# Optimization experiments

Measured on AMD Instinct MI355X. Metric: run time of the kernel, lower is better.

Reference implementation:

```python
import math
import jax, jax.numpy as jnp
import numpy as np

B, L, D, H = 4, 1024, 512, 8
DK = D // H

def setup_inputs() -> dict:
    key = jax.random.key(0)
    ks = jax.random.split(key, 12)
    s = 0.02
    return {
        "query": jax.random.normal(ks[0], (B, L, D), jnp.float32),
        "key": jax.random.normal(ks[1], (B, L, D), jnp.float32),
        "value": jax.random.normal(ks[2], (B, L, D), jnp.float32),
        "wq_w": jax.random.normal(ks[3], (D, D), jnp.float32) * s,
        "wq_b": jnp.zeros((D,), jnp.float32),
        "wk_w": jax.random.normal(ks[4], (D, D), jnp.float32) * s,
        "wk_b": jnp.zeros((D,), jnp.float32),
        "wv_w": jax.random.normal(ks[5], (D, D), jnp.float32) * s,
        "wv_b": jnp.zeros((D,), jnp.float32),
        "dense_w": jax.random.normal(ks[6], (D, D), jnp.float32) * s,
        "dense_b": jnp.zeros((D,), jnp.float32),
        "gate_w": jax.random.normal(ks[7], (D, 1), jnp.float32) * s,
        "gate_b": jnp.zeros((1,), jnp.float32),
        "mp_wq_w": jax.random.normal(ks[8], (D, D), jnp.float32) * s,
        "mp_wq_b": jnp.zeros((D,), jnp.float32),
        "mp_wk_w": jax.random.normal(ks[9], (D, D), jnp.float32) * s,
        "mp_wk_b": jnp.zeros((D,), jnp.float32),
    }

def reference(query, key, value, wq_w, wq_b, wk_w, wk_b, wv_w, wv_b,
              dense_w, dense_b, gate_w, gate_b,
              mp_wq_w, mp_wq_b, mp_wk_w, mp_wk_b):
    # Multi-head projections -> (B, H, L, DK)
    q = (query @ wq_w + wq_b).reshape(B, L, H, DK).transpose(0, 2, 1, 3)
    k = (key @ wk_w + wk_b).reshape(B, L, H, DK).transpose(0, 2, 1, 3)
    v = (value @ wv_w + wv_b).reshape(B, L, H, DK).transpose(0, 2, 1, 3)

    # MaskPerturbation on original (unprojected-into-heads) Q, K; scale by sqrt(d_model)
    qp = query @ mp_wq_w + mp_wq_b              # (B, L, D)
    kp = key @ mp_wk_w + mp_wk_b                # (B, L, D)
    m = jax.nn.sigmoid(jnp.einsum('bqd,bkd->bqk', qp, kp) / math.sqrt(D))  # (B, L, L)

    # Scaled dot-product attention (no mask)
    scores = jnp.einsum('bhqd,bhkd->bhqk', q, k) / math.sqrt(DK)  # (B, H, L, L)
    p_attn = jax.nn.softmax(scores, axis=-1)

    # Calibration: attn_cal = attn * exp(1 - m), combined with per-query gate, re-softmax
    attn_cal = p_attn * jnp.exp(1.0 - m[:, None])                 # (B, H, L, L)
    g = jax.nn.sigmoid(query @ gate_w + gate_b)[:, None]          # (B, 1, L, 1)
    attn_comb = g * p_attn + (1.0 - g) * attn_cal
    attn_final = jax.nn.softmax(attn_comb, axis=-1)

    out = jnp.einsum('bhqk,bhkd->bhqd', attn_final, v)            # (B, H, L, DK)
    out = out.transpose(0, 2, 1, 3).reshape(B, L, D)
    out = out @ dense_w + dense_b                                 # dropout p=0 (eval)
    return (out, m)
```

## Files before the change

### kernel.cpp

```cpp
#include <hip/hip_runtime.h>

#define B_  4
#define L_  1024
#define D_  512
#define H_  8
#define DK_ 64
#define BL_ (B_*L_)

typedef unsigned short us16;
typedef __attribute__((ext_vector_type(8))) short bf16x8;
typedef __attribute__((ext_vector_type(4))) float f32x4;

__device__ __forceinline__ float us2f(us16 u) {
  union { unsigned int i; float f; } x;
  x.i = ((unsigned int)u) << 16;
  return x.f;
}
__device__ __forceinline__ us16 f2us(float f) {
  union { float f; unsigned int i; } x;
  x.f = f;
  unsigned int r = x.i + 0x7FFFu + ((x.i >> 16) & 1u);
  return (us16)(r >> 16);
}
__device__ __forceinline__ us16 cvt_us(float f) { return f2us(f); }
__device__ __forceinline__ us16 cvt_us(us16 u) { return u; }
__device__ __forceinline__ float fexp2(float x) {
  return __builtin_amdgcn_exp2f(x);
}

#define MFMA(a, b, c) __builtin_amdgcn_mfma_f32_16x16x32_bf16(a, b, c, 0, 0, 0)

struct WT6 {
  const float* src[6];
  us16* dst[6];
};
__global__ __launch_bounds__(256) void prep(WT6 p, const float* __restrict__ query,
    const float* __restrict__ gw, const float* __restrict__ gb,
    float* __restrict__ g, us16* __restrict__ qb) {
  __shared__ us16 T[64][72];
  int id = blockIdx.x;
  const int t = threadIdx.x;
  if (id < 1024) {
    int row = id * 4 + (t >> 6);
    int lane = t & 63;
    float pz = 0.f;
    for (int d = lane; d < D_; d += 64) pz += query[(size_t)row * D_ + d] * gw[d];
#pragma unroll
    for (int off = 32; off; off >>= 1) pz += __shfl_down(pz, off);
    if (lane == 0) g[row] = 1.f / (1.f + __expf(-(pz + gb[0])));
    return;
  }
  if (id >= 1408) {
    size_t base = (size_t)(id - 1408) * 4096 + t * 16;
    const float* src = query + base;
    union { bf16x8 v; us16 u[8]; } a0, a1;
#pragma unroll
    for (int j = 0; j < 8; ++j) { a0.u[j] = f2us(src[j]); a1.u[j] = f2us(src[8 + j]); }
    *(bf16x8*)&qb[base] = a0.v;
    *(bf16x8*)&qb[base + 8] = a1.v;
    return;
  }
  id -= 1024;
  const int z = id >> 6;
  const int k0 = ((id >> 3) & 7) * 64, n0 = (id & 7) * 64;
  const float* __restrict__ W = p.src[z];
  us16* __restrict__ Wt = p.dst[z];
  {
    int r = t >> 2, c = (t & 3) * 16;
    const float* src = W + (size_t)(k0 + r) * 512 + n0 + c;
    union { bf16x8 v; us16 u[8]; } p0, p1;
#pragma unroll
    for (int j = 0; j < 8; ++j) { p0.u[j] = f2us(src[j]); p1.u[j] = f2us(src[8 + j]); }
    *(bf16x8*)&T[r][c] = p0.v;
    *(bf16x8*)&T[r][c + 8] = p1.v;
  }
  __syncthreads();
  {
    int n = t >> 2, c = (t & 3) * 16;
    union { bf16x8 v; us16 u[8]; } p0, p1;
#pragma unroll
    for (int j = 0; j < 8; ++j) { p0.u[j] = T[c + j][n]; p1.u[j] = T[c + 8 + j][n]; }
    us16* dst = Wt + (size_t)(n0 + n) * 512 + k0 + c;
    *(bf16x8*)dst = p0.v;
    *(bf16x8*)(dst + 8) = p1.v;
  }
}

__global__ __launch_bounds__(256) void gate_kernel(
    const float* __restrict__ query, const float* __restrict__ gw,
    const float* __restrict__ gb, float* __restrict__ g) {
  int row = blockIdx.x * 4 + (threadIdx.x >> 6);
  int lane = threadIdx.x & 63;
  float p = 0.f;
  for (int d = lane; d < D_; d += 64) p += query[(size_t)row * D_ + d] * gw[d];
#pragma unroll
  for (int off = 32; off; off >>= 1) p += __shfl_down(p, off);
  if (lane == 0) g[row] = 1.f / (1.f + __expf(-(p + gb[0])));
}

struct GJob {
  const float* A; const us16* Ab; const us16* Wt;
  const float* bias; us16* C; int mode; int atype;
};
struct GJobs { GJob j[3]; };

__global__ __launch_bounds__(256) void gemm3(GJobs jobs) {
  __shared__ us16 Al[64][72];
  __shared__ us16 Wl[64][72];
  int f = blockIdx.x + 8 * (blockIdx.y + 64 * blockIdx.z);
  const int cpx = 64 * (int)gridDim.z;
  f = (f & 7) * cpx + (f >> 3);
  const int bx = f & 7, by = (f >> 3) & 63, bz = f >> 9;
  const GJob J = jobs.j[bz];
  const int tid = threadIdx.x;
  const int w = tid >> 6, lane = tid & 63;
  const int quad = lane >> 4, lc = lane & 15;
  const int row0 = by * 64, col0 = bx * 64;
  const int sr = tid >> 2, sc = (tid & 3) * 16;
  f32x4 acc[4] = {};
  for (int k0 = 0; k0 < 512; k0 += 64) {
    if (J.atype) {
      const us16* as = J.Ab + (size_t)(row0 + sr) * 512 + k0 + sc;
      *(bf16x8*)&Al[sr][sc] = *(const bf16x8*)as;
      *(bf16x8*)&Al[sr][sc + 8] = *(const bf16x8*)(as + 8);
    } else {
      const float* as = J.A + (size_t)(row0 + sr) * 512 + k0 + sc;
      union { bf16x8 v; us16 u[8]; } p0, p1;
#pragma unroll
      for (int j = 0; j < 8; ++j) { p0.u[j] = f2us(as[j]); p1.u[j] = f2us(as[8 + j]); }
      *(bf16x8*)&Al[sr][sc] = p0.v;
      *(bf16x8*)&Al[sr][sc + 8] = p1.v;
    }
    {
      const us16* wsrc = J.Wt + (size_t)(col0 + sr) * 512 + k0 + sc;
      *(bf16x8*)&Wl[sr][sc] = *(const bf16x8*)wsrc;
      *(bf16x8*)&Wl[sr][sc + 8] = *(const bf16x8*)(wsrc + 8);
    }
    __syncthreads();
    bf16x8 a0 = *(const bf16x8*)&Al[w * 16 + lc][quad * 8];
    bf16x8 a1 = *(const bf16x8*)&Al[w * 16 + lc][32 + quad * 8];
#pragma unroll
    for (int ct = 0; ct < 4; ++ct) {
      bf16x8 b0 = *(const bf16x8*)&Wl[ct * 16 + lc][quad * 8];
      bf16x8 b1 = *(const bf16x8*)&Wl[ct * 16 + lc][32 + quad * 8];
      acc[ct] = MFMA(a0, b0, acc[ct]);
      acc[ct] = MFMA(a1, b1, acc[ct]);
    }
    __syncthreads();
  }
  const int orow = row0 + w * 16 + quad * 4;
#pragma unroll
  for (int ct = 0; ct < 4; ++ct) {
    const int col = col0 + ct * 16 + lc;
    const float bv = J.bias[col];
    if (J.mode == 0) {
#pragma unroll
      for (int r = 0; r < 4; ++r)
        J.C[(size_t)(orow + r) * 512 + col] = f2us(acc[ct][r] + bv);
    } else {
      const int h = col >> 6, dk = col & 63;
#pragma unroll
      for (int r = 0; r < 4; ++r) {
        const int grow = orow + r;
        const int b = grow >> 10, kv = grow & 1023;
        J.C[(((size_t)b * H_ + h) * DK_ + dk) * L_ + kv] = f2us(acc[ct][r] + bv);
      }
    }
  }
}

__global__ __launch_bounds__(256) void gemm_dense(
    const us16* __restrict__ A, const us16* __restrict__ Wt,
    const float* __restrict__ bias, float* __restrict__ C) {
  __shared__ us16 Al[64][72];
  __shared__ us16 Wl[64][72];
  int f = blockIdx.x + 8 * blockIdx.y;
  f = (f & 7) * 64 + (f >> 3);
  const int bx = f & 7, by = f >> 3;
  const int tid = threadIdx.x;
  const int w = tid >> 6, lane = tid & 63;
  const int quad = lane >> 4, lc = lane & 15;
  const int row0 = by * 64, col0 = bx * 64;
  const int sr = tid >> 2, sc = (tid & 3) * 16;
  f32x4 acc[4] = {};
  for (int k0 = 0; k0 < 512; k0 += 64) {
    const us16* as = A + (size_t)(row0 + sr) * 512 + k0 + sc;
    const us16* wsrc = Wt + (size_t)(col0 + sr) * 512 + k0 + sc;
    *(bf16x8*)&Al[sr][sc] = *(const bf16x8*)as;
    *(bf16x8*)&Al[sr][sc + 8] = *(const bf16x8*)(as + 8);
    *(bf16x8*)&Wl[sr][sc] = *(const bf16x8*)wsrc;
    *(bf16x8*)&Wl[sr][sc + 8] = *(const bf16x8*)(wsrc + 8);
    __syncthreads();
    bf16x8 a0 = *(const bf16x8*)&Al[w * 16 + lc][quad * 8];
    bf16x8 a1 = *(const bf16x8*)&Al[w * 16 + lc][32 + quad * 8];
#pragma unroll
    for (int ct = 0; ct < 4; ++ct) {
      bf16x8 b0 = *(const bf16x8*)&Wl[ct * 16 + lc][quad * 8];
      bf16x8 b1 = *(const bf16x8*)&Wl[ct * 16 + lc][32 + quad * 8];
      acc[ct] = MFMA(a0, b0, acc[ct]);
      acc[ct] = MFMA(a1, b1, acc[ct]);
    }
    __syncthreads();
  }
  const int orow = row0 + w * 16 + quad * 4;
#pragma unroll
  for (int ct = 0; ct < 4; ++ct) {
    const int col = col0 + ct * 16 + lc;
    const float bv = bias[col];
#pragma unroll
    for (int r = 0; r < 4; ++r)
      C[(size_t)(orow + r) * 512 + col] = acc[ct][r] + bv;
  }
}

template <bool WK>
__global__ __launch_bounds__(256) void mask16(
    const us16* __restrict__ QP, const us16* __restrict__ KP,
    float* __restrict__ Mout, const float* __restrict__ gbuf,
    us16* __restrict__ Wk) {
  __shared__ us16 Al[64][72];
  __shared__ us16 Bl[64][72];
  int f = blockIdx.x + 16 * (blockIdx.y + 16 * blockIdx.z);
  f = (f & 7) * 128 + (f >> 3);
  const int bx = f & 15, by = (f >> 4) & 15, b = f >> 8;
  const int tid = threadIdx.x;
  const int w = tid >> 6, lane = tid & 63;
  const int quad = lane >> 4, lc = lane & 15;
  const int row0 = by * 64, col0 = bx * 64;
  const us16* Ab = QP + (size_t)b * L_ * D_;
  const us16* Bb = KP + (size_t)b * L_ * D_;
  const int sr = tid >> 2, sc = (tid & 3) * 16;
  f32x4 acc[4] = {};
  for (int k0 = 0; k0 < 512; k0 += 64) {
    {
      const us16* as = Ab + (size_t)(row0 + sr) * 512 + k0 + sc;
      *(bf16x8*)&Al[sr][sc] = *(const bf16x8*)as;
      *(bf16x8*)&Al[sr][sc + 8] = *(const bf16x8*)(as + 8);
    }
    {
      const us16* bs = Bb + (size_t)(col0 + sr) * 512 + k0 + sc;
      *(bf16x8*)&Bl[sr][sc] = *(const bf16x8*)bs;
      *(bf16x8*)&Bl[sr][sc + 8] = *(const bf16x8*)(bs + 8);
    }
    __syncthreads();
    bf16x8 a0 = *(const bf16x8*)&Al[w * 16 + lc][quad * 8];
    bf16x8 a1 = *(const bf16x8*)&Al[w * 16 + lc][32 + quad * 8];
#pragma unroll
    for (int ct = 0; ct < 4; ++ct) {
      bf16x8 b0 = *(const bf16x8*)&Bl[ct * 16 + lc][quad * 8];
      bf16x8 b1 = *(const bf16x8*)&Bl[ct * 16 + lc][32 + quad * 8];
      acc[ct] = MFMA(a0, b0, acc[ct]);
      acc[ct] = MFMA(a1, b1, acc[ct]);
    }
    __syncthreads();
  }
  const float sc2 = 0.04419417382415922f;
  const int orow = row0 + w * 16 + quad * 4;
  float gq[4];
  if (WK) {
#pragma unroll
    for (int r = 0; r < 4; ++r) gq[r] = gbuf[b * L_ + orow + r];
  }
#pragma unroll
  for (int ct = 0; ct < 4; ++ct) {
    const int col = col0 + ct * 16 + lc;
#pragma unroll
    for (int r = 0; r < 4; ++r) {
      float x = acc[ct][r] * sc2;
      float v = 1.f / (1.f + __expf(-x));
      size_t idx = ((size_t)b * L_ + orow + r) * L_ + col;
      Mout[idx] = v;
      if (WK) Wk[idx] = f2us(gq[r] + (1.f - gq[r]) * __expf(1.f - v));
    }
  }
}

__global__ __launch_bounds__(256, 4) void attn5(
    const us16* Qp, const us16* __restrict__ Kp,
    const us16* __restrict__ Vt, const us16* __restrict__ Wk, us16* O) {
  __shared__ us16 P[16 * 1032];
  __shared__ float red[2][4][16];
  const int tid = threadIdx.x;
  const int w = tid >> 6, lane = tid & 63;
  const int quad = lane >> 4, lc = lane & 15;
  int raw = blockIdx.x + 64 * (blockIdx.y + 8 * blockIdx.z);
  const int c = raw & 7;
  const int rest = raw >> 3;
  const int gg = c * 4 + (rest & 3);
  const int q0 = (rest >> 2) * 16;
  const int h = gg & 7, b = gg >> 3;

  const us16* qptr = Qp + (size_t)(b * L_ + q0 + lc) * D_ + h * DK_;
  bf16x8 qa0 = *(const bf16x8*)(qptr + quad * 8);
  bf16x8 qa1 = *(const bf16x8*)(qptr + 32 + quad * 8);

  const us16* Kbase = Kp + (size_t)b * L_ * D_ + h * DK_;
  const float c1 = 0.18033688011112042f;

  float s[16][4];
  float sm[4] = {0.f, 0.f, 0.f, 0.f};
#pragma unroll
  for (int kt = 0; kt < 16; ++kt) {
    const us16* kr = Kbase + (size_t)(kt * 64 + w * 16 + lc) * D_;
    bf16x8 b0 = *(const bf16x8*)(kr + quad * 8);
    bf16x8 b1 = *(const bf16x8*)(kr + 32 + quad * 8);
    f32x4 a = {};
    __builtin_amdgcn_s_setprio(1);
    a = MFMA(qa0, b0, a);
    a = MFMA(qa1, b1, a);
    __builtin_amdgcn_s_setprio(0);
#pragma unroll
    for (int r = 0; r < 4; ++r) {
      float e = fexp2(a[r] * c1);
      s[kt][r] = e;
      sm[r] += e;
    }
  }
#pragma unroll
  for (int r = 0; r < 4; ++r)
#pragma unroll
    for (int off = 1; off < 16; off <<= 1) sm[r] += __shfl_xor(sm[r], off);
  if (lc == 0)
#pragma unroll
    for (int r = 0; r < 4; ++r) red[0][w][quad * 4 + r] = sm[r];
  __syncthreads();
  float invr[4];
#pragma unroll
  for (int r = 0; r < 4; ++r) {
    const int row = quad * 4 + r;
    invr[r] = 1.44269504088896341f /
              (red[0][0][row] + red[0][1][row] + red[0][2][row] + red[0][3][row]);
  }

  const us16* wkb = Wk + (size_t)(b * L_ + q0 + quad * 4) * L_ + w * 16 + lc;
  float ts[4] = {0.f, 0.f, 0.f, 0.f};
#pragma unroll
  for (int kt = 0; kt < 16; ++kt) {
#pragma unroll
    for (int r = 0; r < 4; ++r) {
      float cv = s[kt][r] * invr[r] * us2f(wkb[(size_t)r * L_ + kt * 64]);
      float e2 = fexp2(cv);
      ts[r] += e2;
      P[(quad * 4 + r) * 1032 + kt * 64 + w * 16 + lc] = f2us(e2);
    }
  }
#pragma unroll
  for (int r = 0; r < 4; ++r)
#pragma unroll
    for (int off = 1; off < 16; off <<= 1) ts[r] += __shfl_xor(ts[r], off);
  if (lc == 0)
#pragma unroll
    for (int r = 0; r < 4; ++r) red[1][w][quad * 4 + r] = ts[r];
  __syncthreads();

  const us16* Vb = Vt + ((size_t)(b * H_ + h) * DK_ + w * 16 + lc) * L_;
  f32x4 oacc = {};
  for (int kv = 0; kv < L_; kv += 32) {
    bf16x8 pa = *(const bf16x8*)&P[lc * 1032 + kv + quad * 8];
    bf16x8 vb = *(const bf16x8*)(Vb + kv + quad * 8);
    __builtin_amdgcn_s_setprio(1);
    oacc = MFMA(pa, vb, oacc);
    __builtin_amdgcn_s_setprio(0);
  }
#pragma unroll
  for (int r = 0; r < 4; ++r) {
    const int row = quad * 4 + r;
    float inv2 = 1.f /
        (red[1][0][row] + red[1][1][row] + red[1][2][row] + red[1][3][row]);
    O[(size_t)(b * L_ + q0 + row) * D_ + h * DK_ + w * 16 + lc] =
        f2us(oacc[r] * inv2);
  }
}

template <int MODE, typename TA>
__global__ __launch_bounds__(256) void gemm16(
    const TA* __restrict__ A, const float* __restrict__ W,
    const float* __restrict__ bias, void* __restrict__ Cout) {
  __shared__ us16 Al[64][56];
  __shared__ us16 Wl[64][56];
  const int tid = threadIdx.x;
  const int w = tid >> 6, lane = tid & 63;
  const int quad = lane >> 4, lc = lane & 15;
  const int row0 = blockIdx.y * 64, col0 = blockIdx.x * 64;
  f32x4 acc[4] = {};
  const int arow = tid >> 2, aks = (tid & 3) * 8;
  const int wk = tid & 31, wns = (tid >> 5) * 8;
  for (int k0 = 0; k0 < 512; k0 += 32) {
    {
      union { bf16x8 v; us16 u[8]; } pk;
      const TA* src = A + (size_t)(row0 + arow) * 512 + k0 + aks;
#pragma unroll
      for (int j = 0; j < 8; ++j) pk.u[j] = cvt_us(src[j]);
      *(bf16x8*)&Al[arow][aks] = pk.v;
    }
    {
      const float* src = W + (size_t)(k0 + wk) * 512 + col0 + wns;
#pragma unroll
      for (int j = 0; j < 8; ++j) Wl[wns + j][wk] = f2us(src[j]);
    }
    __syncthreads();
    bf16x8 af = *(const bf16x8*)&Al[w * 16 + lc][quad * 8];
#pragma unroll
    for (int ct = 0; ct < 4; ++ct) {
      bf16x8 bf = *(const bf16x8*)&Wl[ct * 16 + lc][quad * 8];
      acc[ct] = MFMA(af, bf, acc[ct]);
    }
    __syncthreads();
  }
  const int orow = row0 + w * 16 + quad * 4;
#pragma unroll
  for (int ct = 0; ct < 4; ++ct) {
    const int col = col0 + ct * 16 + lc;
    const float bv = bias[col];
    if (MODE == 0) {
      us16* C = (us16*)Cout;
#pragma unroll
      for (int r = 0; r < 4; ++r)
        C[(size_t)(orow + r) * 512 + col] = f2us(acc[ct][r] + bv);
    } else if (MODE == 1) {
      us16* C = (us16*)Cout;
      const int h = col >> 6, dk = col & 63;
#pragma unroll
      for (int r = 0; r < 4; ++r) {
        const int grow = orow + r;
        const int b = grow >> 10, kv = grow & 1023;
        C[(((size_t)b * H_ + h) * DK_ + dk) * L_ + kv] = f2us(acc[ct][r] + bv);
      }
    } else {
      float* C = (float*)Cout;
#pragma unroll
      for (int r = 0; r < 4; ++r)
        C[(size_t)(orow + r) * 512 + col] = acc[ct][r] + bv;
    }
  }
}

__global__ __launch_bounds__(256, 3) void attn2_fb(
    const us16* Qp, const us16* __restrict__ Kp,
    const us16* __restrict__ Vt, const float* __restrict__ Mm,
    const float* __restrict__ gbuf, us16* O) {
  __shared__ us16 Ql[16][72];
  __shared__ us16 P[16 * 1032];
  __shared__ float red[2][4][16];
  const int tid = threadIdx.x;
  const int w = tid >> 6, lane = tid & 63;
  const int quad = lane >> 4, lc = lane & 15;
  const int b = blockIdx.z, h = blockIdx.y, q0 = blockIdx.x * 16;
  if (tid < 128) {
    int r = tid >> 3, ks = (tid & 7) * 8;
    *(bf16x8*)&Ql[r][ks] =
        *(const bf16x8*)(Qp + (size_t)(b * L_ + q0 + r) * D_ + h * DK_ + ks);
  }
  __syncthreads();
  bf16x8 qa0 = *(const bf16x8*)&Ql[lc][quad * 8];
  bf16x8 qa1 = *(const bf16x8*)&Ql[lc][32 + quad * 8];
  const us16* Kbase = Kp + (size_t)b * L_ * D_ + h * DK_;
  float s[16][4];
#pragma unroll
  for (int kt = 0; kt < 16; ++kt) {
    const us16* kr = Kbase + (size_t)(kt * 64 + w * 16 + lc) * D_;
    bf16x8 b0 = *(const bf16x8*)(kr + quad * 8);
    bf16x8 b1 = *(const bf16x8*)(kr + 32 + quad * 8);
    f32x4 a = {};
    a = MFMA(qa0, b0, a);
    a = MFMA(qa1, b1, a);
#pragma unroll
    for (int r = 0; r < 4; ++r) s[kt][r] = a[r] * 0.125f;
  }
  float sm[4];
#pragma unroll
  for (int r = 0; r < 4; ++r) {
    float t = 0.f;
#pragma unroll
    for (int kt = 0; kt < 16; ++kt) { s[kt][r] = __expf(s[kt][r]); t += s[kt][r]; }
#pragma unroll
    for (int off = 1; off < 16; off <<= 1) t += __shfl_xor(t, off);
    sm[r] = t;
  }
  if (lc == 0)
#pragma unroll
    for (int r = 0; r < 4; ++r) red[0][w][quad * 4 + r] = sm[r];
  __syncthreads();
  float inv[4];
#pragma unroll
  for (int r = 0; r < 4; ++r) {
    const int row = quad * 4 + r;
    inv[r] = 1.f / (red[0][0][row] + red[0][1][row] + red[0][2][row] + red[0][3][row]);
  }
  float gq[4];
#pragma unroll
  for (int r = 0; r < 4; ++r) gq[r] = gbuf[b * L_ + q0 + quad * 4 + r];
#pragma unroll
  for (int r = 0; r < 4; ++r) {
    const float* mrow = Mm + (size_t)(b * L_ + q0 + quad * 4 + r) * L_;
    float t = 0.f;
#pragma unroll
    for (int kt = 0; kt < 16; ++kt) {
      float mval = mrow[kt * 64 + w * 16 + lc];
      float c = s[kt][r] * inv[r] * (gq[r] + (1.f - gq[r]) * __expf(1.f - mval));
      float e = __expf(c);
      s[kt][r] = e;
      t += e;
    }
#pragma unroll
    for (int off = 1; off < 16; off <<= 1) t += __shfl_xor(t, off);
    sm[r] = t;
  }
  if (lc == 0)
#pragma unroll
    for (int r = 0; r < 4; ++r) red[1][w][quad * 4 + r] = sm[r];
  __syncthreads();
#pragma unroll
  for (int r = 0; r < 4; ++r) {
    const int row = quad * 4 + r;
    inv[r] = 1.f / (red[1][0][row] + red[1][1][row] + red[1][2][row] + red[1][3][row]);
  }
#pragma unroll
  for (int kt = 0; kt < 16; ++kt)
#pragma unroll
    for (int r = 0; r < 4; ++r)
      P[(quad * 4 + r) * 1032 + kt * 64 + w * 16 + lc] = f2us(s[kt][r] * inv[r]);
  __syncthreads();
  const us16* Vb = Vt + (size_t)(b * H_ + h) * DK_ * L_;
  f32x4 oacc = {};
  for (int kv = 0; kv < L_; kv += 32) {
    bf16x8 pa = *(const bf16x8*)&P[lc * 1032 + kv + quad * 8];
    bf16x8 vb = *(const bf16x8*)(Vb + (size_t)(w * 16 + lc) * L_ + kv + quad * 8);
    oacc = MFMA(pa, vb, oacc);
  }
#pragma unroll
  for (int r = 0; r < 4; ++r)
    O[(size_t)(b * L_ + q0 + quad * 4 + r) * D_ + h * DK_ + w * 16 + lc] =
        f2us(oacc[r]);
}

extern "C" void kernel_launch(void* const* d_in, const int* in_sizes, int n_in,
                              void* d_out, int out_size, void* d_ws, size_t ws_size,
                              hipStream_t stream) {
  const float* query   = (const float*)d_in[0];
  const float* key     = (const float*)d_in[1];
  const float* value   = (const float*)d_in[2];
  const float* wq_w    = (const float*)d_in[3];
  const float* wq_b    = (const float*)d_in[4];
  const float* wk_w    = (const float*)d_in[5];
  const float* wk_b    = (const float*)d_in[6];
  const float* wv_w    = (const float*)d_in[7];
  const float* wv_b    = (const float*)d_in[8];
  const float* dense_w = (const float*)d_in[9];
  const float* dense_b = (const float*)d_in[10];
  const float* gate_w  = (const float*)d_in[11];
  const float* gate_b  = (const float*)d_in[12];
  const float* mp_wq_w = (const float*)d_in[13];
  const float* mp_wq_b = (const float*)d_in[14];
  const float* mp_wk_w = (const float*)d_in[15];
  const float* mp_wk_b = (const float*)d_in[16];

  const size_t RSZ = (size_t)BL_ * D_;
  const size_t WSZ = (size_t)D_ * D_;
  us16* R0 = (us16*)d_ws;
  us16* R1 = R0 + RSZ;

  float* out0 = (float*)d_out;
  float* outm = out0 + (size_t)B_ * L_ * D_;
  us16*  Vt   = (us16*)d_out;

  dim3 blk(256);

  if (ws_size >= ((size_t)20 << 20)) {
    us16* Wt0 = R1 + RSZ;
    us16* mpq_t = Wt0;
    us16* mpk_t = Wt0 + WSZ;
    us16* wq_t  = Wt0 + 2 * WSZ;
    us16* wk_t  = Wt0 + 3 * WSZ;
    us16* wv_t  = Wt0 + 4 * WSZ;
    us16* dw_t  = Wt0 + 5 * WSZ;
    us16* Wk    = Wt0 + 6 * WSZ;
    float* gbuf = (float*)(Wk + (size_t)B_ * L_ * L_);
    us16* qb = (us16*)((char*)d_out + (4u << 20));

    WT6 wt;
    wt.src[0] = mp_wq_w; wt.dst[0] = mpq_t;
    wt.src[1] = mp_wk_w; wt.dst[1] = mpk_t;
    wt.src[2] = wq_w;    wt.dst[2] = wq_t;
    wt.src[3] = wk_w;    wt.dst[3] = wk_t;
    wt.src[4] = wv_w;    wt.dst[4] = wv_t;
    wt.src[5] = dense_w; wt.dst[5] = dw_t;
    hipLaunchKernelGGL(prep, dim3(1920), blk, 0, stream, wt, query, gate_w, gate_b, gbuf, qb);

    GJobs mp;
    mp.j[0] = { nullptr, qb, mpq_t, mp_wq_b, R0, 0, 1 };
    mp.j[1] = { key, nullptr, mpk_t, mp_wk_b, R1, 0, 0 };
    mp.j[2] = mp.j[1];
    hipLaunchKernelGGL(gemm3, dim3(8, 64, 2), blk, 0, stream, mp);
    hipLaunchKernelGGL(mask16<true>, dim3(16, 16, B_), blk, 0, stream,
                       R0, R1, outm, gbuf, Wk);

    GJobs qkv;
    qkv.j[0] = { nullptr, qb, wq_t, wq_b, R0, 0, 1 };
    qkv.j[1] = { key, nullptr, wk_t, wk_b, R1, 0, 0 };
    qkv.j[2] = { value, nullptr, wv_t, wv_b, Vt, 1, 0 };
    hipLaunchKernelGGL(gemm3, dim3(8, 64, 3), blk, 0, stream, qkv);

    hipLaunchKernelGGL(attn5, dim3(L_ / 16, H_, B_), blk, 0, stream, R0, R1, Vt, Wk, R0);
    hipLaunchKernelGGL(gemm_dense, dim3(8, 64), blk, 0, stream, R0, dw_t, dense_b, out0);
  } else {
    float* gbuf = (float*)((char*)d_out + (4u << 20));
    dim3 gproj(8, 64);
    hipLaunchKernelGGL((gemm16<0, float>), gproj, blk, 0, stream, query, mp_wq_w, mp_wq_b, (void*)R0);
    hipLaunchKernelGGL((gemm16<0, float>), gproj, blk, 0, stream, key,   mp_wk_w, mp_wk_b, (void*)R1);
    hipLaunchKernelGGL(mask16<false>, dim3(16, 16, B_), blk, 0, stream,
                       R0, R1, outm, (const float*)nullptr, (us16*)nullptr);
    hipLaunchKernelGGL((gemm16<0, float>), gproj, blk, 0, stream, query, wq_w, wq_b, (void*)R0);
    hipLaunchKernelGGL((gemm16<0, float>), gproj, blk, 0, stream, key,   wk_w, wk_b, (void*)R1);
    hipLaunchKernelGGL((gemm16<1, float>), gproj, blk, 0, stream, value, wv_w, wv_b, (void*)Vt);
    hipLaunchKernelGGL(gate_kernel, dim3(BL_ / 4), blk, 0, stream, query, gate_w, gate_b, gbuf);
    hipLaunchKernelGGL(attn2_fb, dim3(L_ / 16, H_, B_), blk, 0, stream, R0, R1, Vt, outm, gbuf, R0);
    hipLaunchKernelGGL((gemm16<2, us16>), gproj, blk, 0, stream, R0, dense_w, dense_b, (void*)out0);
  }
}
```

Baseline: 241.4 us.

## Stage K tiles into LDS with async global_load_lds, four-deep pipeline

The attention kernel's QK^T phase now copies K tiles from global memory straight into shared memory with global_load_lds, using a 4-stage ring buffer and an XOR swizzle. Explicit vmcnt waits and sched barriers replace the direct global register loads. The aim is to hide global-load latency behind the MFMA and exp work. The ring reuses the P shared buffer, which risks hazards with later uses of P, and the fixed scheduling limits how the compiler can reorder instructions.

```diff
diff --git a/kernel.cpp b/kernel.cpp
--- a/kernel.cpp
+++ b/kernel.cpp
@@ -275,7 +275,10 @@
   }
 }
 
-__global__ __launch_bounds__(256, 4) void attn5(
+typedef const __attribute__((address_space(1))) unsigned int* gas_u32;
+typedef __attribute__((address_space(3))) unsigned int* las_u32;
+
+__global__ __launch_bounds__(256, 4) void attn8(
     const us16* Qp, const us16* __restrict__ Kp,
     const us16* __restrict__ Vt, const us16* __restrict__ Wk, us16* O) {
   __shared__ us16 P[16 * 1032];
@@ -295,15 +298,37 @@
   bf16x8 qa1 = *(const bf16x8*)(qptr + 32 + quad * 8);
 
   const us16* Kbase = Kp + (size_t)b * L_ * D_ + h * DK_;
+  const int srow = lane >> 3;
+  const int sblk = ((lane & 7) ^ srow) * 8;
+  us16* kst = &P[w * 4096];
+
+  auto stage = [&](int kt, int d) {
+#pragma unroll
+    for (int i = 0; i < 2; ++i) {
+      const us16* src =
+          Kbase + (size_t)(kt * 64 + w * 16 + i * 8 + srow) * D_ + sblk;
+      __builtin_amdgcn_global_load_lds(
+          (gas_u32)src, (las_u32)(kst + d * 1024 + i * 512), 16, 0, 0);
+    }
+  };
+
   const float c1 = 0.18033688011112042f;
+
+  stage(0, 0); stage(1, 1); stage(2, 2); stage(3, 3);
 
   float s[16][4];
   float sm[4] = {0.f, 0.f, 0.f, 0.f};
 #pragma unroll
   for (int kt = 0; kt < 16; ++kt) {
-    const us16* kr = Kbase + (size_t)(kt * 64 + w * 16 + lc) * D_;
-    bf16x8 b0 = *(const bf16x8*)(kr + quad * 8);
-    bf16x8 b1 = *(const bf16x8*)(kr + 32 + quad * 8);
+    const int d = kt & 3;
+    if (kt <= 12)      asm volatile("s_waitcnt vmcnt(6)" ::: "memory");
+    else if (kt == 13) asm volatile("s_waitcnt vmcnt(4)" ::: "memory");
+    else if (kt == 14) asm volatile("s_waitcnt vmcnt(2)" ::: "memory");
+    else               asm volatile("s_waitcnt vmcnt(0)" ::: "memory");
+    __builtin_amdgcn_sched_barrier(0);
+    bf16x8 b0 = *(const bf16x8*)&kst[d * 1024 + lc * 64 + ((quad ^ (lc & 7)) * 8)];
+    bf16x8 b1 = *(const bf16x8*)&kst[d * 1024 + lc * 64 + (((4 + quad) ^ (lc & 7)) * 8)];
+    if (kt + 4 < 16) stage(kt + 4, d);
     f32x4 a = {};
     __builtin_amdgcn_s_setprio(1);
     a = MFMA(qa0, b0, a);
@@ -315,6 +340,7 @@
       s[kt][r] = e;
       sm[r] += e;
     }
+    __builtin_amdgcn_sched_barrier(0);
   }
 #pragma unroll
   for (int r = 0; r < 4; ++r)
@@ -601,7 +627,7 @@
     qkv.j[2] = { value, nullptr, wv_t, wv_b, Vt, 1, 0 };
     hipLaunchKernelGGL(gemm3, dim3(8, 64, 3), blk, 0, stream, qkv);
 
-    hipLaunchKernelGGL(attn5, dim3(L_ / 16, H_, B_), blk, 0, stream, R0, R1, Vt, Wk, R0);
+    hipLaunchKernelGGL(attn8, dim3(L_ / 16, H_, B_), blk, 0, stream, R0, R1, Vt, Wk, R0);
     hipLaunchKernelGGL(gemm_dense, dim3(8, 64), blk, 0, stream, R0, dw_t, dense_b, out0);
   } else {
     float* gbuf = (float*)((char*)d_out + (4u << 20));
```

Result: faster. 222.1 us (-8.0%).
